# Optimization experiments

Hardware: AMD Instinct MI355X
Metric: run time of the kernel (lower is better)

Reference implementation:

```python
import jax, jax.numpy as jnp
import numpy as np

BSZ, SL, K, D_IN, D_OUT = 2, 1024, 24, 512, 512
K_U, K_Y = 3, 2
USE_HANKEL_L = False


def get_top_eigh(l, k, use_hankel_L):
    i = np.arange(1, l + 1, dtype=np.float64)
    s = i[:, None] + i[None, :]
    if use_hankel_L:
        Z = ((-1.0) ** (s - 2.0) + 1.0) * 8.0 / ((s + 3.0) * (s - 1.0) * (s + 1.0))
    else:
        Z = 2.0 / (s ** 3 - s)
    sigma, phi = np.linalg.eigh(Z)  # ascending
    return jnp.asarray(sigma[-k:], jnp.float32), jnp.asarray(phi[:, -k:], jnp.float32)


def shift(x, k):
    # causal shift along time axis 1, zero-padded at the front
    if k == 0:
        return x
    return jnp.pad(x, ((0, 0), (k, 0), (0, 0)))[:, : x.shape[1]]


def fft_causal_conv(filters, u):
    # filters: (l, k); u: (b, l, d) -> (b, l, k, d) causal convolution per filter
    l = u.shape[1]
    n = 2 * l
    F = jnp.fft.rfft(filters, n=n, axis=0)  # (n//2+1, k)
    U = jnp.fft.rfft(u, n=n, axis=1)        # (b, n//2+1, d)
    Y = jnp.fft.irfft(U[:, :, None, :] * F[None, :, :, None], n=n, axis=1)
    return Y[:, :l].astype(u.dtype)


def compute_ar_u(M_u, u):
    # ar_u[b,t,o] = sum_{i<k_u} M_u[i] @ u_{t-i}
    U = jnp.stack([shift(u, i) for i in range(M_u.shape[0])])  # (k_u, b, l, d_in)
    return jnp.einsum('koi,kbli->blo', M_u, U)


def compute_spectral(u, sigma, phi, M_phi_plus, M_phi_minus, m_y):
    l = u.shape[1]
    phi_s = phi * sigma ** 0.25  # eigenvalue-scaled spectral filters (l, k)
    U_plus = fft_causal_conv(phi_s, u)  # (b, l, k, d_in)
    spec = jnp.einsum('blki,koi->blo', U_plus, M_phi_plus)
    if not USE_HANKEL_L:
        # negative-featurization branch: filters modulated by (-1)^i
        alt = ((-1.0) ** jnp.arange(l)).astype(u.dtype)
        U_minus = fft_causal_conv(phi_s * alt[:, None], u)
        spec = spec + jnp.einsum('blki,koi->blo', U_minus, M_phi_minus)
    if m_y is not None:
        spec = shift(spec, m_y.shape[0])  # spectral features enter at lag k_y (paper: t-2)
    return spec


def compute_ar_y(m_y, y):
    # true short linear recurrence on outputs:
    # yhat_t = y_t + sum_{i=1}^{k_y} m_y[i-1] @ yhat_{t-i}; returns the correction term
    k_y, d_out = m_y.shape[0], m_y.shape[1]
    b = y.shape[0]

    def step(carry, y_t):  # carry: (k_y, b, d_out) = [yhat_{t-1}, ..., yhat_{t-k_y}]
        ar_t = jnp.einsum('koj,kbj->bo', m_y, carry)
        yhat_t = y_t + ar_t
        carry = jnp.concatenate([yhat_t[None], carry[:-1]], axis=0)
        return carry, ar_t

    y_tl = jnp.swapaxes(y, 0, 1)  # (l, b, d_out)
    _, ar = jax.lax.scan(step, jnp.zeros((k_y, b, d_out), y.dtype), y_tl)
    return jnp.swapaxes(ar, 0, 1)


def setup_inputs() -> dict:
    key = jax.random.key(0)
    k0, k1, k2, k3, k4 = jax.random.split(key, 5)
    inputs = jax.random.normal(k0, (BSZ, SL, D_IN), jnp.float32)
    M_u = jax.random.normal(k1, (K_U, D_OUT, D_IN), jnp.float32) * 0.02
    M_phi_plus = jax.random.normal(k2, (K, D_OUT, D_IN), jnp.float32) * 0.02
    M_phi_minus = jax.random.normal(k3, (K, D_OUT, D_IN), jnp.float32) * 0.02
    m_y = jax.random.normal(k4, (K_Y, D_OUT, D_OUT), jnp.float32) * 0.02
    sigma, phi = get_top_eigh(SL, K, USE_HANKEL_L)
    return {'inputs': inputs, 'M_u': M_u, 'M_phi_plus': M_phi_plus,
            'M_phi_minus': M_phi_minus, 'm_y': m_y, 'sigma': sigma, 'phi': phi}


def reference(inputs, M_u, M_phi_plus, M_phi_minus, m_y, sigma, phi):
    ar_u = compute_ar_u(M_u, inputs)
    spectral = compute_spectral(inputs, sigma, phi, M_phi_plus, M_phi_minus, m_y)
    y_t = ar_u + spectral
    y_t = y_t + compute_ar_y(m_y, y_t)  # learnable_m_y=True branch
    return y_t  # dropout p=0.0 (identity)
```

## Files before the change

### kernel.cpp

```cpp
#include <hip/hip_runtime.h>
#include <hip/hip_bf16.h>


typedef unsigned short u16;
typedef __attribute__((ext_vector_type(8))) short  vshort8;
typedef __attribute__((ext_vector_type(4))) short  vshort4;
typedef __attribute__((ext_vector_type(4))) float  f32x4;
typedef __attribute__((ext_vector_type(4))) unsigned int vuint4;

__device__ __forceinline__ u16 f2b(float x) {
  __hip_bfloat16 h = __float2bfloat16(x);
  return __builtin_bit_cast(u16, h);
}
__device__ __forceinline__ float b2f(u16 x) {
  unsigned int u = ((unsigned int)x) << 16;
  return __builtin_bit_cast(float, u);
}

struct GB {
  const u16* A; const u16* B;
  float* Cf; u16* Cb;
  const float* zf; float* out;
  u16* A2T; u16* Au;
  int M, N;
};

template<int V>
__global__ __launch_bounds__(256) void g2(GB a) {
  const int tid = threadIdx.x;
  int bn = blockIdx.x, bm = blockIdx.y;
  const int bz = blockIdx.z;
  int cj = 0, cb = 0, cd = 0, chh = 0;
  if (V == 1) {
    int p = blockIdx.x;
    bm = (int)((sqrtf(8.f * (float)p + 1.f) - 1.f) * 0.5f);
    cj = p - (bm * (bm + 1)) / 2;
    bn = blockIdx.y;
    cb = bz >> 1; chh = bz & 1; cd = bm - cj;
  }
  const int m0 = bm * 128, n0 = bn * 128;
  __shared__ u16 lA[4096], lB[4096];
  f32x4 acc[4][4];
#pragma unroll
  for (int i = 0; i < 4; i++)
#pragma unroll
    for (int j = 0; j < 4; j++) acc[i][j] = f32x4{0.f, 0.f, 0.f, 0.f};

  int kbeg = 0, kend = 0;
  if (V == 0) kend = 512;
  if (V == 1) { kbeg = chh * 3072; kend = kbeg + 3072; }
  if (V == 2) {
    int jmax = (m0 >> 6) + 1;
    kbeg = bz * 2048;
    kend = kbeg + 2048;
    int tk = (jmax + 1) * 512;
    if (kend > tk) kend = tk;
    if (kend < kbeg) kend = kbeg;
  }
  if (V == 3 || V == 5 || V == 6 || V == 7) kend = 1024;

  const int lane = tid & 63, wv = tid >> 6, wr = wv >> 1, wc = wv & 1;
  const u16* Ap = a.A;
  if (V == 5) Ap = a.A + (size_t)bz * 524288;

  for (int k0 = kbeg; k0 < kend; k0 += 32) {
#pragma unroll
    for (int it = 0; it < 2; ++it) {
      int q = tid + it * 256;
      int r = q >> 2, cq = q & 3;
      int kk = k0 + cq * 8;
      vuint4 v;
      if (V == 0) {
        v = *(const vuint4*)(Ap + (size_t)(m0 + r) * 512 + kk);
      } else if (V == 1) {
        v = *(const vuint4*)(Ap + (size_t)cd * 786432 + (size_t)r * 6144 + kk);
      } else if (V == 2) {
        int m = m0 + r, j = m >> 6, b = (m >> 5) & 1, c = m & 31;
        int tau = kk >> 9, p = kk & 511;
        if (tau > j) v = vuint4{0u, 0u, 0u, 0u};
        else v = *(const vuint4*)(Ap + (size_t)(b * 1024 + c * 32 + j - tau) * 512 + p);
      } else if (V == 3) {
        int m = m0 + r;
        if (m < a.M) v = *(const vuint4*)(Ap + (size_t)m * 1024 + kk);
        else v = vuint4{0u, 0u, 0u, 0u};
      } else if (V == 5) {
        v = *(const vuint4*)(Ap + (size_t)(m0 + r) * 1024 + kk);
      } else if (V == 6) {
        if (r < 64) v = *(const vuint4*)(Ap + (size_t)r * 1024 + kk);
        else v = vuint4{0u, 0u, 0u, 0u};
      } else {
        if (r < 32) {
          int b = r & 1, k2 = r >> 1;
          v = *(const vuint4*)(Ap + (size_t)(b * 32 + 2 * k2) * 1024 + kk);
        } else v = vuint4{0u, 0u, 0u, 0u};
      }
      *(vuint4*)(&lA[(((r >> 4) * 4 + cq) * 16 + (r & 15)) * 8]) = v;

      int n = n0 + r;
      vuint4 w;
      if (V == 0) {
        w = *(const vuint4*)(a.B + (size_t)n * 512 + kk);
      } else if (V == 1) {
        int kh = kk >> 7, sp = kk & 127;
        w = *(const vuint4*)(a.B + (size_t)(cb * 512 + n) * 49152 + kh * 1024 + cj * 128 + sp);
      } else if (V == 2) {
        int tau = kk >> 9, p = kk & 511;
        w = *(const vuint4*)(a.B + (size_t)tau * 524288 + (size_t)n * 1024 + p);
      } else if (V == 3) {
        int jn = n >> 9, o = n & 511;
        w = *(const vuint4*)(a.B + (size_t)(jn + 1) * 524288 + (size_t)o * 1024 + kk);
      } else if (V == 5) {
        w = *(const vuint4*)(a.B + (size_t)n * 1024 + kk);
      } else {
        const u16* src = (n < 512)
            ? (a.B + (size_t)32 * 524288 + (size_t)n * 1024 + kk)
            : (a.B + (size_t)31 * 524288 + (size_t)(n - 512) * 1024 + kk);
        w = *(const vuint4*)src;
      }
      *(vuint4*)(&lB[(((r >> 4) * 4 + cq) * 16 + (r & 15)) * 8]) = w;
    }
    __syncthreads();
    vshort8 af[4], bf_[4];
#pragma unroll
    for (int s = 0; s < 4; s++) {
      af[s]  = *(const vshort8*)&lA[(((wr * 4 + s) * 4 + (lane >> 4)) * 16 + (lane & 15)) * 8];
      bf_[s] = *(const vshort8*)&lB[(((wc * 4 + s) * 4 + (lane >> 4)) * 16 + (lane & 15)) * 8];
    }
#pragma unroll
    for (int i = 0; i < 4; i++)
#pragma unroll
      for (int j = 0; j < 4; j++)
        acc[i][j] = __builtin_amdgcn_mfma_f32_16x16x32_bf16(af[i], bf_[j], acc[i][j], 0, 0, 0);
    __syncthreads();
  }

#pragma unroll
  for (int i = 0; i < 4; i++) {
    int em = m0 + wr * 64 + i * 16 + ((lane >> 4) << 2);
#pragma unroll
    for (int j = 0; j < 4; j++) {
      int n = n0 + wc * 64 + j * 16 + (lane & 15);
      f32x4 v = acc[i][j];
      if (V == 0) {
        int b = em >> 10, s = em & 1023;
        if (n < 24576) {
          int kh = n >> 9, o = n & 511;
          vshort4 pk = { (short)f2b(v[0]), (short)f2b(v[1]), (short)f2b(v[2]), (short)f2b(v[3]) };
          *(vshort4*)(&a.A2T[(size_t)(b * 512 + o) * 49152 + (size_t)kh * 1024 + s]) = pk;
        } else {
          int jj = (n - 24576) >> 9, o = n & 511;
#pragma unroll
          for (int t = 0; t < 4; t++)
            a.Au[((size_t)(b * 3 + jj) * 1024 + (s + t)) * 512 + o] = f2b(v[t]);
        }
      } else if (V == 1) {
        float* C = a.Cf + (size_t)(cb * 16 + chh * 8 + cj) * 524288;
#pragma unroll
        for (int t = 0; t < 4; t++) C[(size_t)(em + t) * 512 + n] = v[t];
      } else if (V == 2) {
        float* C = a.Cf + (size_t)bz * 1048576;
#pragma unroll
        for (int t = 0; t < 4; t++) C[(size_t)(em + t) * 512 + n] = v[t];
      } else if (V == 3) {
        int jj = n >> 9, oo = n & 511;
#pragma unroll
        for (int t = 0; t < 4; t++) {
          int m = em + t;
          if (m < a.M) {
            int b = m >> 5, c = m & 31;
            float zv = a.zf[(size_t)(jj * 64 + b * 32 + c) * 512 + oo];
            a.out[(size_t)b * 524288 + (size_t)(c * 32 + jj) * 512 + oo] = v[t] + zv;
          }
        }
      } else if (V == 5) {
        u16* C = a.Cb + (size_t)bz * 524288;
#pragma unroll
        for (int t = 0; t < 4; t++) C[(size_t)(em + t) * 1024 + n] = f2b(v[t]);
      } else if (V == 6) {
        int jrow = (n < 512) ? 31 : 30, oo = n & 511;
#pragma unroll
        for (int t = 0; t < 4; t++) {
          int m = em + t;
          if (m < 62) {
            int b = m & 1, c = m >> 1;
            a.Cf[(size_t)m * 1024 + n] =
                v[t] + a.zf[(size_t)(jrow * 64 + b * 32 + (c + 1)) * 512 + oo];
          }
        }
      } else {
        int jrow = (n < 512) ? 31 : 30, oo = n & 511;
#pragma unroll
        for (int t = 0; t < 4; t++) {
          int m = em + t;
          if (m < 32) {
            int b = m & 1, k2 = m >> 1;
            float val = v[t] + a.zf[(size_t)(jrow * 64 + b * 32 + 2 * k2) * 512 + oo];
            a.Cb[(size_t)(b * 32 + 2 * k2 + 1) * 1024 + n] = f2b(val);
          }
        }
      }
    }
  }
}

__global__ void k_prep_X(const float* __restrict__ u, u16* __restrict__ X, int n) {
  int i = blockIdx.x * 256 + threadIdx.x;
  if (i < n) X[i] = f2b(u[i]);
}

__global__ void k_prep_phis(const float* __restrict__ phi, const float* __restrict__ sigma,
                            float* __restrict__ phis) {
  int i = blockIdx.x * 256 + threadIdx.x;
  if (i >= 1024 * 48) return;
  int tau = i / 48, kf = i % 48, k = (kf >= 24) ? kf - 24 : kf;
  float v = phi[tau * 24 + k] * powf(sigma[k], 0.25f);
  if (kf >= 24 && (tau & 1)) v = -v;
  phis[i] = v;
}

__global__ void k_prep_W1(const float* __restrict__ Mp, const float* __restrict__ Mm,
                          const float* __restrict__ Mu, u16* __restrict__ W1) {
  int i = blockIdx.x * 256 + threadIdx.x;
  if (i >= 13369344) return;
  float v;
  if (i < 6291456) v = Mp[i];
  else if (i < 12582912) v = Mm[i - 6291456];
  else v = Mu[i - 12582912];
  W1[i] = f2b(v);
}

__global__ void k_prep_Wtoep(const float* __restrict__ phis, u16* __restrict__ W) {
  int i = blockIdx.x * 256 + threadIdx.x;
  if (i >= 6291456) return;
  int kap = i % 6144, row = i / 6144;
  int tp = row & 127, d = row >> 7;
  int kh = kap >> 7, sp = kap & 127;
  int tau = d * 128 + tp - sp;
  W[i] = (tau >= 0 && tau < 1024) ? f2b(phis[tau * 48 + kh]) : (u16)0;
}

__global__ void k_initTop(const float* __restrict__ my, u16* __restrict__ Top) {
  int i = blockIdx.x * 256 + threadIdx.x;
  if (i >= 1048576) return;
  int mat = i >> 19, rem = i & 524287, o = rem >> 10, k = rem & 1023;
  u16 v;
  if (mat == 0) v = (k == o) ? (u16)0x3F80 : (u16)0;
  else v = (k < 512) ? f2b(my[o * 512 + k]) : f2b(my[262144 + o * 512 + (k - 512)]);
  Top[i] = v;
}

__global__ __launch_bounds__(256) void k_transT(const u16* __restrict__ Top,
                                                u16* __restrict__ STc, int c) {
  __shared__ u16 tile[64][72];
  int tx = blockIdx.x, ty = blockIdx.y;
  int tid = threadIdx.x;
  int r = tid >> 2, seg = tid & 3;
  int k = ty * 64 + r;
  const u16* src = (k < 512) ? Top + (size_t)c * 524288 + (size_t)k * 1024 + tx * 64
                             : Top + (size_t)(c - 1) * 524288 + (size_t)(k - 512) * 1024 + tx * 64;
  *(vuint4*)&tile[r][seg * 16]     = *(const vuint4*)(src + seg * 16);
  *(vuint4*)&tile[r][seg * 16 + 8] = *(const vuint4*)(src + seg * 16 + 8);
  __syncthreads();
  int n = tx * 64 + r;
  u16 tmp[16];
#pragma unroll
  for (int j = 0; j < 16; j++) tmp[j] = tile[seg * 16 + j][r];
  *(vuint4*)&STc[(size_t)n * 1024 + ty * 64 + seg * 16]     = *(vuint4*)&tmp[0];
  *(vuint4*)&STc[(size_t)n * 1024 + ty * 64 + seg * 16 + 8] = *(vuint4*)&tmp[8];
}

__global__ void k_combine(const float* __restrict__ parts, const u16* __restrict__ Au,
                          u16* __restrict__ ybf) {
  int i = blockIdx.x * 256 + threadIdx.x;
  if (i >= 1048576) return;
  int b = i >> 19, rest = i & 524287, t = rest >> 9, o = rest & 511;
  float y = 0.f;
#pragma unroll
  for (int j = 0; j < 3; j++)
    if (t >= j) y += b2f(Au[((size_t)(b * 3 + j) * 1024 + (t - j)) * 512 + o]);
  if (t >= 2) {
    int tp = t - 2, bmv = tp >> 7;
    size_t e = (size_t)tp * 512 + o;
    for (int j = 0; j <= bmv; ++j)
      y += parts[(size_t)(b * 16 + j) * 524288 + e] +
           parts[(size_t)(b * 16 + 8 + j) * 524288 + e];
  }
  ybf[i] = f2b(y);
}

__global__ void k_zreduce(const float* __restrict__ zp, float* __restrict__ z) {
  int i = blockIdx.x * 256 + threadIdx.x;
  if (i >= 1048576) return;
  float s = 0.f;
#pragma unroll
  for (int j = 0; j < 8; j++) s += zp[(size_t)j * 1048576 + i];
  z[i] = s;
}

__global__ void k_wm(const float* __restrict__ zf, u16* __restrict__ Wm) {
  int i = blockIdx.x * 256 + threadIdx.x;
  if (i >= 65536) return;
  int row = i >> 10, n = i & 1023;
  int b = row & 1, c = row >> 1;
  int jrow = (n < 512) ? 31 : 30, oo = n & 511;
  Wm[i] = f2b(zf[(size_t)(jrow * 64 + b * 32 + c) * 512 + oo]);
}

__global__ __launch_bounds__(256) void k_bnd2(const u16* __restrict__ Top,
                                              const float* __restrict__ ubuf,
                                              float* __restrict__ bnd,
                                              u16* __restrict__ Abnd, int k) {
  __shared__ float st[2048];
  int tid = threadIdx.x;
  const float* s0 = bnd + (size_t)k * 2048;
  for (int j = tid; j < 2048; j += 256) st[j] = s0[j];
  __syncthreads();
  int q4 = blockIdx.x * 256 + tid;
  int q = q4 >> 2, quarter = q4 & 3;
  int b = q >> 10, kk = q & 1023;
  const u16* row = (kk < 512) ? Top + (size_t)64 * 524288 + (size_t)kk * 1024
                              : Top + (size_t)63 * 524288 + (size_t)(kk - 512) * 1024;
  const float* stb = st + b * 1024 + quarter * 256;
  const u16* rp = row + quarter * 256;
  float sum = 0.f;
  for (int t = 0; t < 32; ++t) {
    vuint4 v = *(const vuint4*)(rp + t * 8);
    const unsigned int* vu = (const unsigned int*)&v;
#pragma unroll
    for (int e = 0; e < 4; ++e) {
      unsigned int pw = vu[e];
      float lo = __builtin_bit_cast(float, (pw & 0xffffu) << 16);
      float hi = __builtin_bit_cast(float, pw & 0xffff0000u);
      sum += lo * stb[t * 8 + e * 2] + hi * stb[t * 8 + e * 2 + 1];
    }
  }
  sum += __shfl_xor(sum, 1);
  sum += __shfl_xor(sum, 2);
  if (quarter == 0) {
    float s = sum + ubuf[(size_t)(4 * k + b) * 1024 + kk];
    bnd[(size_t)(k + 1) * 2048 + b * 1024 + kk] = s;
    Abnd[(size_t)(b * 32 + 2 * k + 2) * 1024 + kk] = f2b(s);
  }
}

extern "C" void kernel_launch(void* const* d_in, const int* in_sizes, int n_in,
                              void* d_out, int out_size, void* d_ws, size_t ws_size,
                              hipStream_t stream) {
  const float* u     = (const float*)d_in[0];
  const float* Mu    = (const float*)d_in[1];
  const float* Mp    = (const float*)d_in[2];
  const float* Mm    = (const float*)d_in[3];
  const float* my    = (const float*)d_in[4];
  const float* sigma = (const float*)d_in[5];
  const float* phi   = (const float*)d_in[6];
  float* out = (float*)d_out;

  char* ws = (char*)d_ws;
  size_t off = 0;
  auto alc = [&](size_t b) { size_t p = off; off = (off + b + 255) & ~(size_t)255; return p; };
  u16*  X     = (u16*)(ws + alc(2097152));
  u16*  Wtoep = (u16*)(ws + alc(12582912));
  u16*  A2T   = (u16*)(ws + alc(100663296));
  u16*  Au    = (u16*)(ws + alc(6291456));
  u16*  W1    = (u16*)(ws + alc(26738688));
  char* ptail = ws + alc(40370176); (void)ptail;
  float* phis = (float*)(ws + alc(196608));
  float* bnd  = (float*)(ws + alc(131072));
  u16*  Abnd  = (u16*)(ws + alc(131072));
  u16*  Wm    = (u16*)(ws + alc(131072));
  float* ubuf = (float*)(ws + alc(262144));
  if (off > ws_size) return;
  float* partsBig = (float*)W1;
  float* zparts   = partsBig;
  u16*  ybf = A2T;
  float* zf = (float*)((char*)A2T + (4 << 20));
  u16*  Top = (u16*)((char*)A2T + (size_t)(8 << 20));
  u16*  STc = (u16*)((char*)A2T + (size_t)(76 << 20));

  k_prep_X<<<dim3(4096), 256, 0, stream>>>(u, X, 1048576);
  k_prep_phis<<<dim3(192), 256, 0, stream>>>(phi, sigma, phis);
  k_prep_W1<<<dim3(52224), 256, 0, stream>>>(Mp, Mm, Mu, W1);
  k_prep_Wtoep<<<dim3(24576), 256, 0, stream>>>(phis, Wtoep);

  {
    GB g{}; g.A = X; g.B = W1; g.A2T = A2T; g.Au = Au; g.M = 2048; g.N = 26112;
    g2<0><<<dim3(204, 16, 1), 256, 0, stream>>>(g);
  }
  {
    GB g{}; g.A = Wtoep; g.B = A2T; g.Cf = partsBig; g.M = 1024; g.N = 512;
    g2<1><<<dim3(36, 4, 4), 256, 0, stream>>>(g);
  }
  k_combine<<<dim3(4096), 256, 0, stream>>>(partsBig, Au, ybf);

  k_initTop<<<dim3(4096), 256, 0, stream>>>(my, Top);
  {
    const int cs[5] = {1, 2, 4, 8, 16};
    for (int li = 0; li < 5; ++li) {
      int c = cs[li];
      k_transT<<<dim3(16, 16), 256, 0, stream>>>(Top, STc, c);
      GB s{}; s.A = Top + 524288; s.B = STc; s.Cb = Top + (size_t)(c + 1) * 524288;
      s.M = 512; s.N = 1024;
      g2<5><<<dim3(8, 4, c), 256, 0, stream>>>(s);
    }
    k_transT<<<dim3(16, 16), 256, 0, stream>>>(Top, STc, 32);
    GB s{}; s.A = Top + (size_t)31 * 524288; s.B = STc;
    s.Cb = Top + (size_t)63 * 524288; s.M = 512; s.N = 1024;
    g2<5><<<dim3(8, 4, 2), 256, 0, stream>>>(s);
  }

  {
    GB g{}; g.A = ybf; g.B = Top; g.Cf = zparts; g.M = 2048; g.N = 512;
    g2<2><<<dim3(4, 16, 8), 256, 0, stream>>>(g);
  }
  k_zreduce<<<dim3(4096), 256, 0, stream>>>(zparts, zf);

  k_wm<<<dim3(256), 256, 0, stream>>>(zf, Wm);
  {
    GB g{}; g.A = Wm; g.B = Top; g.Cf = ubuf; g.zf = zf; g.M = 64; g.N = 1024;
    g2<6><<<dim3(8, 1, 1), 256, 0, stream>>>(g);
  }
  hipMemsetAsync(bnd, 0, 8192, stream);
  hipMemsetAsync(Abnd, 0, 131072, stream);
  for (int k = 0; k < 15; ++k)
    k_bnd2<<<dim3(32), 256, 0, stream>>>(Top, ubuf, bnd, Abnd, k);
  {
    GB g{}; g.A = Abnd; g.B = Top; g.Cb = Abnd; g.zf = zf; g.M = 32; g.N = 1024;
    g2<7><<<dim3(8, 1, 1), 256, 0, stream>>>(g);
  }

  {
    GB g{}; g.A = Abnd; g.B = Top; g.zf = zf; g.out = out; g.M = 64; g.N = 16384;
    g2<3><<<dim3(128, 1, 1), 256, 0, stream>>>(g);
  }
}
```

Baseline: 779.1 us.

## Use direct global-to-LDS loads, bf16 partials, and rebalanced Toeplitz GEMM split

```diff
diff --git a/kernel.cpp b/kernel.cpp
--- a/kernel.cpp
+++ b/kernel.cpp
@@ -17,11 +17,18 @@
   return __builtin_bit_cast(float, u);
 }
 
+__device__ __forceinline__ void gll16(const u16* g, u16* l) {
+  __builtin_amdgcn_global_load_lds((__attribute__((address_space(1))) void*)g,
+                                   (__attribute__((address_space(3))) void*)l,
+                                   16, 0, 0);
+}
+
 struct GB {
   const u16* A; const u16* B;
   float* Cf; u16* Cb;
   const float* zf; float* out;
   u16* A2T; u16* Au;
+  const u16* zp;
   int M, N;
 };
 
@@ -30,25 +37,20 @@
   const int tid = threadIdx.x;
   int bn = blockIdx.x, bm = blockIdx.y;
   const int bz = blockIdx.z;
-  int cj = 0, cb = 0, cd = 0, chh = 0;
+  int cj = 0, cb = 0, cd = 0, slot = 0;
+  int kbeg = 0, kend = 0;
+  if (V == 0) { bm = blockIdx.x; bn = blockIdx.y; kend = 512; }
   if (V == 1) {
-    int p = blockIdx.x;
-    bm = (int)((sqrtf(8.f * (float)p + 1.f) - 1.f) * 0.5f);
-    cj = p - (bm * (bm + 1)) / 2;
-    bn = blockIdx.y;
-    cb = bz >> 1; chh = bz & 1; cd = bm - cj;
+    int rest = blockIdx.x; bm = blockIdx.y;
+    bn = rest & 3; cj = (rest >> 2) & 7;
+    int chcb = rest >> 5;
+    cd = bm - cj;
+    if (cd < 0) return;
+    cb = chcb & 1;
+    slot = (chcb << 3) | cj;
+    kbeg = (chcb >> 1) * 1536; kend = kbeg + 1536;
   }
   const int m0 = bm * 128, n0 = bn * 128;
-  __shared__ u16 lA[4096], lB[4096];
-  f32x4 acc[4][4];
-#pragma unroll
-  for (int i = 0; i < 4; i++)
-#pragma unroll
-    for (int j = 0; j < 4; j++) acc[i][j] = f32x4{0.f, 0.f, 0.f, 0.f};
-
-  int kbeg = 0, kend = 0;
-  if (V == 0) kend = 512;
-  if (V == 1) { kbeg = chh * 3072; kend = kbeg + 3072; }
   if (V == 2) {
     int jmax = (m0 >> 6) + 1;
     kbeg = bz * 2048;
@@ -59,65 +61,69 @@
   }
   if (V == 3 || V == 5 || V == 6 || V == 7) kend = 1024;
 
+  __shared__ u16 lA[4096], lB[4096];
+  f32x4 acc[4][4];
+#pragma unroll
+  for (int i = 0; i < 4; i++)
+#pragma unroll
+    for (int j = 0; j < 4; j++) acc[i][j] = f32x4{0.f, 0.f, 0.f, 0.f};
+
   const int lane = tid & 63, wv = tid >> 6, wr = wv >> 1, wc = wv & 1;
   const u16* Ap = a.A;
   if (V == 5) Ap = a.A + (size_t)bz * 524288;
+  const u16* zp = a.zp + lane * 8;
 
   for (int k0 = kbeg; k0 < kend; k0 += 32) {
 #pragma unroll
     for (int it = 0; it < 2; ++it) {
-      int q = tid + it * 256;
-      int r = q >> 2, cq = q & 3;
-      int kk = k0 + cq * 8;
-      vuint4 v;
+      const int weff = wv + it * 4;
+      const int lrow = weff * 16 + (lane & 15);
+      const int kk = k0 + ((lane >> 4) << 3);
+      const u16* ga;
       if (V == 0) {
-        v = *(const vuint4*)(Ap + (size_t)(m0 + r) * 512 + kk);
+        ga = Ap + (size_t)(m0 + lrow) * 512 + kk;
       } else if (V == 1) {
-        v = *(const vuint4*)(Ap + (size_t)cd * 786432 + (size_t)r * 6144 + kk);
+        ga = Ap + (size_t)cd * 786432 + (size_t)lrow * 6144 + kk;
       } else if (V == 2) {
-        int m = m0 + r, j = m >> 6, b = (m >> 5) & 1, c = m & 31;
+        int m = m0 + lrow, j = m >> 6, b = (m >> 5) & 1, c = m & 31;
         int tau = kk >> 9, p = kk & 511;
-        if (tau > j) v = vuint4{0u, 0u, 0u, 0u};
-        else v = *(const vuint4*)(Ap + (size_t)(b * 1024 + c * 32 + j - tau) * 512 + p);
+        ga = (tau > j) ? zp
+                       : Ap + (size_t)(b * 1024 + c * 32 + j - tau) * 512 + p;
       } else if (V == 3) {
-        int m = m0 + r;
-        if (m < a.M) v = *(const vuint4*)(Ap + (size_t)m * 1024 + kk);
-        else v = vuint4{0u, 0u, 0u, 0u};
+        int m = m0 + lrow;
+        ga = (m < a.M) ? Ap + (size_t)m * 1024 + kk : zp;
       } else if (V == 5) {
-        v = *(const vuint4*)(Ap + (size_t)(m0 + r) * 1024 + kk);
+        ga = Ap + (size_t)(m0 + lrow) * 1024 + kk;
       } else if (V == 6) {
-        if (r < 64) v = *(const vuint4*)(Ap + (size_t)r * 1024 + kk);
-        else v = vuint4{0u, 0u, 0u, 0u};
+        ga = (lrow < 64) ? Ap + (size_t)lrow * 1024 + kk : zp;
       } else {
-        if (r < 32) {
-          int b = r & 1, k2 = r >> 1;
-          v = *(const vuint4*)(Ap + (size_t)(b * 32 + 2 * k2) * 1024 + kk);
-        } else v = vuint4{0u, 0u, 0u, 0u};
+        if (lrow < 32) {
+          int b = lrow & 1, k2 = lrow >> 1;
+          ga = Ap + (size_t)(b * 32 + 2 * k2) * 1024 + kk;
+        } else ga = zp;
       }
-      *(vuint4*)(&lA[(((r >> 4) * 4 + cq) * 16 + (r & 15)) * 8]) = v;
-
-      int n = n0 + r;
-      vuint4 w;
+      gll16(ga, &lA[weff * 512]);
+      const int n = n0 + lrow;
+      const u16* gb;
       if (V == 0) {
-        w = *(const vuint4*)(a.B + (size_t)n * 512 + kk);
+        gb = a.B + (size_t)n * 512 + kk;
       } else if (V == 1) {
         int kh = kk >> 7, sp = kk & 127;
-        w = *(const vuint4*)(a.B + (size_t)(cb * 512 + n) * 49152 + kh * 1024 + cj * 128 + sp);
+        gb = a.B + (size_t)(cb * 512 + n) * 49152 + kh * 1024 + cj * 128 + sp;
       } else if (V == 2) {
         int tau = kk >> 9, p = kk & 511;
-        w = *(const vuint4*)(a.B + (size_t)tau * 524288 + (size_t)n * 1024 + p);
+        gb = a.B + (size_t)tau * 524288 + (size_t)n * 1024 + p;
       } else if (V == 3) {
         int jn = n >> 9, o = n & 511;
-        w = *(const vuint4*)(a.B + (size_t)(jn + 1) * 524288 + (size_t)o * 1024 + kk);
+        gb = a.B + (size_t)(jn + 1) * 524288 + (size_t)o * 1024 + kk;
       } else if (V == 5) {
-        w = *(const vuint4*)(a.B + (size_t)n * 1024 + kk);
+        gb = a.B + (size_t)n * 1024 + kk;
       } else {
-        const u16* src = (n < 512)
-            ? (a.B + (size_t)32 * 524288 + (size_t)n * 1024 + kk)
-            : (a.B + (size_t)31 * 524288 + (size_t)(n - 512) * 1024 + kk);
-        w = *(const vuint4*)src;
+        gb = (n < 512)
+            ? a.B + (size_t)32 * 524288 + (size_t)n * 1024 + kk
+            : a.B + (size_t)31 * 524288 + (size_t)(n - 512) * 1024 + kk;
       }
-      *(vuint4*)(&lB[(((r >> 4) * 4 + cq) * 16 + (r & 15)) * 8]) = w;
+      gll16(gb, &lB[weff * 512]);
     }
     __syncthreads();
     vshort8 af[4], bf_[4];
@@ -154,9 +160,9 @@
             a.Au[((size_t)(b * 3 + jj) * 1024 + (s + t)) * 512 + o] = f2b(v[t]);
         }
       } else if (V == 1) {
-        float* C = a.Cf + (size_t)(cb * 16 + chh * 8 + cj) * 524288;
-#pragma unroll
-        for (int t = 0; t < 4; t++) C[(size_t)(em + t) * 512 + n] = v[t];
+        u16* C = a.Cb + (size_t)slot * 524288;
+#pragma unroll
+        for (int t = 0; t < 4; t++) C[(size_t)(em + t) * 512 + n] = f2b(v[t]);
       } else if (V == 2) {
         float* C = a.Cf + (size_t)bz * 1048576;
 #pragma unroll
@@ -269,23 +275,41 @@
   *(vuint4*)&STc[(size_t)n * 1024 + ty * 64 + seg * 16 + 8] = *(vuint4*)&tmp[8];
 }
 
-__global__ void k_combine(const float* __restrict__ parts, const u16* __restrict__ Au,
+__device__ __forceinline__ void addp(float* acc, vuint4 v) {
+  const unsigned int* vu = (const unsigned int*)&v;
+#pragma unroll
+  for (int e = 0; e < 4; ++e) {
+    unsigned int pw = vu[e];
+    acc[2 * e]     += __builtin_bit_cast(float, (pw & 0xffffu) << 16);
+    acc[2 * e + 1] += __builtin_bit_cast(float, pw & 0xffff0000u);
+  }
+}
+
+__global__ void k_combine(const u16* __restrict__ parts, const u16* __restrict__ Au,
                           u16* __restrict__ ybf) {
   int i = blockIdx.x * 256 + threadIdx.x;
-  if (i >= 1048576) return;
-  int b = i >> 19, rest = i & 524287, t = rest >> 9, o = rest & 511;
-  float y = 0.f;
+  if (i >= 131072) return;
+  int og = i & 63, t = (i >> 6) & 1023, b = i >> 16;
+  float acc[8];
+#pragma unroll
+  for (int e = 0; e < 8; ++e) acc[e] = 0.f;
 #pragma unroll
   for (int j = 0; j < 3; j++)
-    if (t >= j) y += b2f(Au[((size_t)(b * 3 + j) * 1024 + (t - j)) * 512 + o]);
+    if (t >= j)
+      addp(acc, *(const vuint4*)(Au + ((size_t)(b * 3 + j) * 1024 + (t - j)) * 512 + og * 8));
   if (t >= 2) {
     int tp = t - 2, bmv = tp >> 7;
-    size_t e = (size_t)tp * 512 + o;
-    for (int j = 0; j <= bmv; ++j)
-      y += parts[(size_t)(b * 16 + j) * 524288 + e] +
-           parts[(size_t)(b * 16 + 8 + j) * 524288 + e];
-  }
-  ybf[i] = f2b(y);
+    for (int g = 0; g < 8; ++g) {
+      const u16* base = parts + (size_t)(b * 0 + g * 8) * 524288 + (size_t)tp * 512 + og * 8;
+      if ((g & 1) != b) continue;
+      for (int j = 0; j <= bmv; ++j)
+        addp(acc, *(const vuint4*)(base + (size_t)j * 524288));
+    }
+  }
+  u16 o16[8];
+#pragma unroll
+  for (int e = 0; e < 8; ++e) o16[e] = f2b(acc[e]);
+  *(vuint4*)(ybf + ((size_t)(b * 1024 + t)) * 512 + og * 8) = *(vuint4*)o16;
 }
 
 __global__ void k_zreduce(const float* __restrict__ zp, float* __restrict__ z) {
@@ -369,28 +393,33 @@
   u16*  Abnd  = (u16*)(ws + alc(131072));
   u16*  Wm    = (u16*)(ws + alc(131072));
   float* ubuf = (float*)(ws + alc(262144));
+  u16*  zpad  = (u16*)(ws + alc(32768));
   if (off > ws_size) return;
-  float* partsBig = (float*)W1;
-  float* zparts   = partsBig;
+  u16*  partsBf = (u16*)W1;
+  float* zparts = (float*)W1;
   u16*  ybf = A2T;
   float* zf = (float*)((char*)A2T + (4 << 20));
   u16*  Top = (u16*)((char*)A2T + (size_t)(8 << 20));
   u16*  STc = (u16*)((char*)A2T + (size_t)(76 << 20));
 
+  hipMemsetAsync(zpad, 0, 32768, stream);
+
   k_prep_X<<<dim3(4096), 256, 0, stream>>>(u, X, 1048576);
   k_prep_phis<<<dim3(192), 256, 0, stream>>>(phi, sigma, phis);
   k_prep_W1<<<dim3(52224), 256, 0, stream>>>(Mp, Mm, Mu, W1);
   k_prep_Wtoep<<<dim3(24576), 256, 0, stream>>>(phis, Wtoep);
 
   {
-    GB g{}; g.A = X; g.B = W1; g.A2T = A2T; g.Au = Au; g.M = 2048; g.N = 26112;
-    g2<0><<<dim3(204, 16, 1), 256, 0, stream>>>(g);
-  }
-  {
-    GB g{}; g.A = Wtoep; g.B = A2T; g.Cf = partsBig; g.M = 1024; g.N = 512;
-    g2<1><<<dim3(36, 4, 4), 256, 0, stream>>>(g);
-  }
-  k_combine<<<dim3(4096), 256, 0, stream>>>(partsBig, Au, ybf);
+    GB g{}; g.A = X; g.B = W1; g.A2T = A2T; g.Au = Au; g.zp = zpad;
+    g.M = 2048; g.N = 26112;
+    g2<0><<<dim3(16, 204, 1), 256, 0, stream>>>(g);
+  }
+  {
+    GB g{}; g.A = Wtoep; g.B = A2T; g.Cb = partsBf; g.zp = zpad;
+    g.M = 1024; g.N = 512;
+    g2<1><<<dim3(256, 8, 1), 256, 0, stream>>>(g);
+  }
+  k_combine<<<dim3(512), 256, 0, stream>>>(partsBf, Au, ybf);
 
   k_initTop<<<dim3(4096), 256, 0, stream>>>(my, Top);
   {
@@ -399,24 +428,25 @@
       int c = cs[li];
       k_transT<<<dim3(16, 16), 256, 0, stream>>>(Top, STc, c);
       GB s{}; s.A = Top + 524288; s.B = STc; s.Cb = Top + (size_t)(c + 1) * 524288;
-      s.M = 512; s.N = 1024;
+      s.zp = zpad; s.M = 512; s.N = 1024;
       g2<5><<<dim3(8, 4, c), 256, 0, stream>>>(s);
     }
     k_transT<<<dim3(16, 16), 256, 0, stream>>>(Top, STc, 32);
     GB s{}; s.A = Top + (size_t)31 * 524288; s.B = STc;
-    s.Cb = Top + (size_t)63 * 524288; s.M = 512; s.N = 1024;
+    s.Cb = Top + (size_t)63 * 524288; s.zp = zpad; s.M = 512; s.N = 1024;
     g2<5><<<dim3(8, 4, 2), 256, 0, stream>>>(s);
   }
 
   {
-    GB g{}; g.A = ybf; g.B = Top; g.Cf = zparts; g.M = 2048; g.N = 512;
+    GB g{}; g.A = ybf; g.B = Top; g.Cf = zparts; g.zp = zpad; g.M = 2048; g.N = 512;
     g2<2><<<dim3(4, 16, 8), 256, 0, stream>>>(g);
   }
   k_zreduce<<<dim3(4096), 256, 0, stream>>>(zparts, zf);
 
   k_wm<<<dim3(256), 256, 0, stream>>>(zf, Wm);
   {
-    GB g{}; g.A = Wm; g.B = Top; g.Cf = ubuf; g.zf = zf; g.M = 64; g.N = 1024;
+    GB g{}; g.A = Wm; g.B = Top; g.Cf = ubuf; g.zf = zf; g.zp = zpad;
+    g.M = 64; g.N = 1024;
     g2<6><<<dim3(8, 1, 1), 256, 0, stream>>>(g);
   }
   hipMemsetAsync(bnd, 0, 8192, stream);
@@ -424,12 +454,14 @@
   for (int k = 0; k < 15; ++k)
     k_bnd2<<<dim3(32), 256, 0, stream>>>(Top, ubuf, bnd, Abnd, k);
   {
-    GB g{}; g.A = Abnd; g.B = Top; g.Cb = Abnd; g.zf = zf; g.M = 32; g.N = 1024;
+    GB g{}; g.A = Abnd; g.B = Top; g.Cb = Abnd; g.zf = zf; g.zp = zpad;
+    g.M = 32; g.N = 1024;
     g2<7><<<dim3(8, 1, 1), 256, 0, stream>>>(g);
   }
 
   {
-    GB g{}; g.A = Abnd; g.B = Top; g.zf = zf; g.out = out; g.M = 64; g.N = 16384;
+    GB g{}; g.A = Abnd; g.B = Top; g.zf = zf; g.out = out; g.zp = zpad;
+    g.M = 64; g.N = 16384;
     g2<3><<<dim3(128, 1, 1), 256, 0, stream>>>(g);
   }
 }
```

Measured after the change: 858.8 us. +10.2%, slower.
